# Kernel tuning notes

Measured on AMD Instinct MI355X. Metric: run time of the kernel, lower is better.

The kernel has to match this reference:

```python
import jax, jax.numpy as jnp
import numpy as np

B, N, E, OD, RD, ED, H = 4, 2048, 8192, 3, 4, 4, 8


def _linear(x, W, b):
    return x @ W + b


def _mlp_rel(x, p):
    # RelationalModel: Lin-ELU-Lin-ELU-Lin-ELU-Lin
    h = jax.nn.elu(_linear(x, p[0], p[1]))
    h = jax.nn.elu(_linear(h, p[2], p[3]))
    h = jax.nn.elu(_linear(h, p[4], p[5]))
    return _linear(h, p[6], p[7])


def _mlp_obj(x, p):
    # ObjectModel: Lin-ELU-Lin-ELU-Lin
    h = jax.nn.elu(_linear(x, p[0], p[1]))
    h = jax.nn.elu(_linear(h, p[2], p[3]))
    return _linear(h, p[4], p[5])


def setup_inputs() -> dict:
    key = jax.random.key(0)
    ks = jax.random.split(key, 24)
    X = jax.random.normal(ks[0], (B, OD, N), jnp.float32)
    Ra = jax.random.normal(ks[1], (B, E, RD), jnp.float32)
    # one-hot incidence matrices (receiver / sender), as in the torch repo
    ro_idx = jax.random.randint(ks[2], (B, E), 0, N)
    ri_idx = jax.random.randint(ks[3], (B, E), 0, N)
    Ro = jax.nn.one_hot(ro_idx, N, dtype=jnp.float32)
    Ri = jax.nn.one_hot(ri_idx, N, dtype=jnp.float32)

    def w(k, i, o):
        return jax.random.normal(k, (i, o), jnp.float32) * (1.0 / np.sqrt(i))

    def b(k, o):
        return jax.random.normal(k, (o,), jnp.float32) * 0.01

    m_in = 2 * OD + RD  # 10
    d = {
        "X": X, "Ra": Ra, "Ro": Ro, "Ri": Ri,
        # phi_R1: m_in -> H -> H -> H -> ED
        "r1W1": w(ks[4], m_in, H), "r1b1": b(ks[5], H),
        "r1W2": w(ks[6], H, H), "r1b2": b(ks[7], H),
        "r1W3": w(ks[8], H, H), "r1b3": b(ks[9], H),
        "r1W4": w(ks[10], H, ED), "r1b4": b(ks[11], ED),
        # phi_R2: m_in -> H -> H -> H -> 1
        "r2W1": w(ks[12], m_in, H), "r2b1": b(ks[13], H),
        "r2W2": w(ks[14], H, H), "r2b2": b(ks[15], H),
        "r2W3": w(ks[16], H, H), "r2b3": b(ks[17], H),
        "r2W4": w(ks[18], H, 1), "r2b4": b(ks[19], 1),
        # phi_O: OD+ED -> H -> H -> 3
        "oW1": w(ks[20], OD + ED, H), "ob1": b(ks[21], H),
        "oW2": w(ks[22], H, H), "ob2": b(ks[23], H),
        "oW3": w(jax.random.fold_in(key, 99), H, 3),
        "ob3": jnp.zeros((3,), jnp.float32),
    }
    return d


def reference(X, Ra, Ro, Ri,
              r1W1, r1b1, r1W2, r1b2, r1W3, r1b3, r1W4, r1b4,
              r2W1, r2b1, r2W2, r2b2, r2W3, r2b3, r2W4, r2b4,
              oW1, ob1, oW2, ob2, oW3, ob3):
    r1 = (r1W1, r1b1, r1W2, r1b2, r1W3, r1b3, r1W4, r1b4)
    r2 = (r2W1, r2b1, r2W2, r2b2, r2W3, r2b3, r2W4, r2b4)
    po = (oW1, ob1, oW2, ob2, oW3, ob3)

    Xt = jnp.swapaxes(X, 1, 2)          # [B, N, OD]
    Xi = jnp.einsum('ben,bnd->bed', Ro, Xt)   # receiver gather [B,E,OD]
    Xo = jnp.einsum('ben,bnd->bed', Ri, Xt)   # sender gather   [B,E,OD]
    m1 = jnp.concatenate([Xi, Xo, Ra], axis=2)  # [B,E,2*OD+RD]
    Eff = _mlp_rel(m1, r1)              # [B,E,ED]
    A = jnp.einsum('ben,bed->bnd', Ri, Eff)     # scatter-add to nodes [B,N,ED]
    C = jnp.concatenate([Xt, A], axis=2)        # [B,N,OD+ED]
    X_tilde = _mlp_obj(C, po)           # [B,N,3]
    Xi_t = jnp.einsum('ben,bnd->bed', Ri, X_tilde)
    Xo_t = jnp.einsum('ben,bnd->bed', Ro, X_tilde)
    m2 = jnp.concatenate([Xi_t, Xo_t, Eff], axis=2)  # [B,E,6+ED]
    W = jax.nn.sigmoid(_mlp_rel(m2, r2))  # [B,E,1]
    return W
```

## Files before the change

### kernel.cpp

```cpp
#include <hip/hip_runtime.h>
#include <hip/hip_bf16.h>
#include <cstdint>

#define NBATCH 4
#define NNODE  2048
#define NEDGE  8192
#define ETOT   (NBATCH * NEDGE)
#define NTOT   (NBATCH * NNODE)

typedef uint32_t u32x4 __attribute__((ext_vector_type(4)));

__device__ __forceinline__ float elu(float x) {
    return x > 0.0f ? x : expm1f(x);
}

__global__ void in_idx_kernel(const u32x4* __restrict__ Ro,
                              const u32x4* __restrict__ Ri,
                              int* __restrict__ ro_idx,
                              int* __restrict__ ri_idx,
                              float* __restrict__ A, int a_elems) {
    const int gtid = blockIdx.x * blockDim.x + threadIdx.x;
    if (gtid < a_elems) A[gtid] = 0.0f;

    const int wid  = gtid >> 6;
    const int lane = threadIdx.x & 63;
    const int nrows = 2 * ETOT;
    if (wid >= nrows) return;

    const bool second = (wid >= ETOT);
    const int  row    = second ? wid - ETOT : wid;
    const u32x4* __restrict__ src = (second ? Ri : Ro) + (size_t)row * (NNODE / 4);
    int* __restrict__ dst = second ? ri_idx : ro_idx;

    #pragma unroll
    for (int c = 0; c < NNODE / 256; ++c) {
        const u32x4 v = __builtin_nontemporal_load(&src[c * 64 + lane]);
        const uint32_t o = v.x | v.y | v.z | v.w;
        const unsigned long long found = __ballot(o != 0u);
        if (found) {
            if (o) {
                const int base = c * 256 + lane * 4;
                if      (v.x) dst[row] = base;
                else if (v.y) dst[row] = base + 1;
                else if (v.z) dst[row] = base + 2;
                else          dst[row] = base + 3;
            }
            break;
        }
    }
}

__global__ void in_edge1_kernel(const float* __restrict__ X,
                                const float* __restrict__ Ra,
                                const int* __restrict__ ro_idx,
                                const int* __restrict__ ri_idx,
                                const float* __restrict__ W1, const float* __restrict__ b1,
                                const float* __restrict__ W2, const float* __restrict__ b2,
                                const float* __restrict__ W3, const float* __restrict__ b3,
                                const float* __restrict__ W4, const float* __restrict__ b4,
                                float* __restrict__ Eff,
                                float* __restrict__ A) {
    __shared__ float sW1[80], sb1[8], sW2[64], sb2[8], sW3[64], sb3[8], sW4[32], sb4[4];
    const int t = threadIdx.x, bs = blockDim.x;
    for (int i = t; i < 80; i += bs) sW1[i] = W1[i];
    for (int i = t; i < 8;  i += bs) sb1[i] = b1[i];
    for (int i = t; i < 64; i += bs) sW2[i] = W2[i];
    for (int i = t; i < 8;  i += bs) sb2[i] = b2[i];
    for (int i = t; i < 64; i += bs) sW3[i] = W3[i];
    for (int i = t; i < 8;  i += bs) sb3[i] = b3[i];
    for (int i = t; i < 32; i += bs) sW4[i] = W4[i];
    for (int i = t; i < 4;  i += bs) sb4[i] = b4[i];
    __syncthreads();

    const int e = blockIdx.x * blockDim.x + threadIdx.x;
    if (e >= ETOT) return;
    const int b  = e >> 13;
    const int ro = ro_idx[e] & (NNODE - 1);
    const int ri = ri_idx[e] & (NNODE - 1);

    float x[10];
    const float* Xb = X + (long)b * 3 * NNODE;
    #pragma unroll
    for (int d = 0; d < 3; ++d) x[d]     = Xb[d * NNODE + ro];
    #pragma unroll
    for (int d = 0; d < 3; ++d) x[3 + d] = Xb[d * NNODE + ri];
    const float4 ra = ((const float4*)Ra)[e];
    x[6] = ra.x; x[7] = ra.y; x[8] = ra.z; x[9] = ra.w;

    float h1[8], h2[8], h3[8];
    #pragma unroll
    for (int j = 0; j < 8; ++j) {
        float s = sb1[j];
        #pragma unroll
        for (int i = 0; i < 10; ++i) s += x[i] * sW1[i * 8 + j];
        h1[j] = elu(s);
    }
    #pragma unroll
    for (int j = 0; j < 8; ++j) {
        float s = sb2[j];
        #pragma unroll
        for (int i = 0; i < 8; ++i) s += h1[i] * sW2[i * 8 + j];
        h2[j] = elu(s);
    }
    #pragma unroll
    for (int j = 0; j < 8; ++j) {
        float s = sb3[j];
        #pragma unroll
        for (int i = 0; i < 8; ++i) s += h2[i] * sW3[i * 8 + j];
        h3[j] = elu(s);
    }
    float* Arow = A + ((long)(b * NNODE + ri)) * 4;
    float4 eff;
    float* effp = (float*)&eff;
    #pragma unroll
    for (int j = 0; j < 4; ++j) {
        float s = sb4[j];
        #pragma unroll
        for (int i = 0; i < 8; ++i) s += h3[i] * sW4[i * 4 + j];
        effp[j] = s;
        atomicAdd(&Arow[j], s);
    }
    ((float4*)Eff)[e] = eff;
}

__global__ void in_node_kernel(const float* __restrict__ X,
                               const float* __restrict__ A,
                               const float* __restrict__ W1, const float* __restrict__ b1,
                               const float* __restrict__ W2, const float* __restrict__ b2,
                               const float* __restrict__ W3, const float* __restrict__ b3,
                               float* __restrict__ Xtil) {
    __shared__ float sW1[56], sb1[8], sW2[64], sb2[8], sW3[24], sb3[3];
    const int t = threadIdx.x, bs = blockDim.x;
    for (int i = t; i < 56; i += bs) sW1[i] = W1[i];
    for (int i = t; i < 8;  i += bs) sb1[i] = b1[i];
    for (int i = t; i < 64; i += bs) sW2[i] = W2[i];
    for (int i = t; i < 8;  i += bs) sb2[i] = b2[i];
    for (int i = t; i < 24; i += bs) sW3[i] = W3[i];
    for (int i = t; i < 3;  i += bs) sb3[i] = b3[i];
    __syncthreads();

    const int n = blockIdx.x * blockDim.x + threadIdx.x;
    if (n >= NTOT) return;
    const int b  = n >> 11;
    const int nn = n & (NNODE - 1);

    float c[7];
    const float* Xb = X + (long)b * 3 * NNODE;
    #pragma unroll
    for (int d = 0; d < 3; ++d) c[d] = Xb[d * NNODE + nn];
    const float4 a4 = ((const float4*)A)[n];
    c[3] = a4.x; c[4] = a4.y; c[5] = a4.z; c[6] = a4.w;

    float h1[8], h2[8];
    #pragma unroll
    for (int j = 0; j < 8; ++j) {
        float s = sb1[j];
        #pragma unroll
        for (int i = 0; i < 7; ++i) s += c[i] * sW1[i * 8 + j];
        h1[j] = elu(s);
    }
    #pragma unroll
    for (int j = 0; j < 8; ++j) {
        float s = sb2[j];
        #pragma unroll
        for (int i = 0; i < 8; ++i) s += h1[i] * sW2[i * 8 + j];
        h2[j] = elu(s);
    }
    #pragma unroll
    for (int j = 0; j < 3; ++j) {
        float s = sb3[j];
        #pragma unroll
        for (int i = 0; i < 8; ++i) s += h2[i] * sW3[i * 3 + j];
        Xtil[(long)n * 3 + j] = s;
    }
}

__global__ void in_edge2_kernel(const float* __restrict__ Xtil,
                                const float* __restrict__ Eff,
                                const int* __restrict__ ro_idx,
                                const int* __restrict__ ri_idx,
                                const float* __restrict__ W1, const float* __restrict__ b1,
                                const float* __restrict__ W2, const float* __restrict__ b2,
                                const float* __restrict__ W3, const float* __restrict__ b3,
                                const float* __restrict__ W4, const float* __restrict__ b4,
                                float* __restrict__ out) {
    __shared__ float sW1[80], sb1[8], sW2[64], sb2[8], sW3[64], sb3[8], sW4[8], sb4[1];
    const int t = threadIdx.x, bs = blockDim.x;
    for (int i = t; i < 80; i += bs) sW1[i] = W1[i];
    for (int i = t; i < 8;  i += bs) sb1[i] = b1[i];
    for (int i = t; i < 64; i += bs) sW2[i] = W2[i];
    for (int i = t; i < 8;  i += bs) sb2[i] = b2[i];
    for (int i = t; i < 64; i += bs) sW3[i] = W3[i];
    for (int i = t; i < 8;  i += bs) sb3[i] = b3[i];
    for (int i = t; i < 8;  i += bs) sW4[i] = W4[i];
    for (int i = t; i < 1;  i += bs) sb4[i] = b4[i];
    __syncthreads();

    const int e = blockIdx.x * blockDim.x + threadIdx.x;
    if (e >= ETOT) return;
    const int b  = e >> 13;
    const int ro = ro_idx[e] & (NNODE - 1);
    const int ri = ri_idx[e] & (NNODE - 1);

    float x[10];
    const float* Xb = Xtil + (long)b * NNODE * 3;
    #pragma unroll
    for (int d = 0; d < 3; ++d) x[d]     = Xb[(long)ri * 3 + d];
    #pragma unroll
    for (int d = 0; d < 3; ++d) x[3 + d] = Xb[(long)ro * 3 + d];
    const float4 ef = ((const float4*)Eff)[e];
    x[6] = ef.x; x[7] = ef.y; x[8] = ef.z; x[9] = ef.w;

    float h1[8], h2[8], h3[8];
    #pragma unroll
    for (int j = 0; j < 8; ++j) {
        float s = sb1[j];
        #pragma unroll
        for (int i = 0; i < 10; ++i) s += x[i] * sW1[i * 8 + j];
        h1[j] = elu(s);
    }
    #pragma unroll
    for (int j = 0; j < 8; ++j) {
        float s = sb2[j];
        #pragma unroll
        for (int i = 0; i < 8; ++i) s += h1[i] * sW2[i * 8 + j];
        h2[j] = elu(s);
    }
    #pragma unroll
    for (int j = 0; j < 8; ++j) {
        float s = sb3[j];
        #pragma unroll
        for (int i = 0; i < 8; ++i) s += h2[i] * sW3[i * 8 + j];
        h3[j] = elu(s);
    }
    float s = sb4[0];
    #pragma unroll
    for (int i = 0; i < 8; ++i) s += h3[i] * sW4[i];
    out[e] = 1.0f / (1.0f + expf(-s));
}

extern "C" void kernel_launch(void* const* d_in, const int* in_sizes, int n_in,
                              void* d_out, int out_size, void* d_ws, size_t ws_size,
                              hipStream_t stream) {
    const float* X  = (const float*)d_in[0];
    const float* Ra = (const float*)d_in[1];
    const float* Ro = (const float*)d_in[2];
    const float* Ri = (const float*)d_in[3];
    const float* r1W1 = (const float*)d_in[4];  const float* r1b1 = (const float*)d_in[5];
    const float* r1W2 = (const float*)d_in[6];  const float* r1b2 = (const float*)d_in[7];
    const float* r1W3 = (const float*)d_in[8];  const float* r1b3 = (const float*)d_in[9];
    const float* r1W4 = (const float*)d_in[10]; const float* r1b4 = (const float*)d_in[11];
    const float* r2W1 = (const float*)d_in[12]; const float* r2b1 = (const float*)d_in[13];
    const float* r2W2 = (const float*)d_in[14]; const float* r2b2 = (const float*)d_in[15];
    const float* r2W3 = (const float*)d_in[16]; const float* r2b3 = (const float*)d_in[17];
    const float* r2W4 = (const float*)d_in[18]; const float* r2b4 = (const float*)d_in[19];
    const float* oW1  = (const float*)d_in[20]; const float* ob1  = (const float*)d_in[21];
    const float* oW2  = (const float*)d_in[22]; const float* ob2  = (const float*)d_in[23];
    const float* oW3  = (const float*)d_in[24]; const float* ob3  = (const float*)d_in[25];

    char* ws = (char*)d_ws;
    int*   ro_idx = (int*)(ws + 0);
    int*   ri_idx = (int*)(ws + 131072);
    float* Eff    = (float*)(ws + 262144);
    float* A      = (float*)(ws + 786432);
    float* Xtil   = (float*)(ws + 917504);

    in_idx_kernel<<<(2 * ETOT * 64) / 256, 256, 0, stream>>>(
        (const u32x4*)Ro, (const u32x4*)Ri, ro_idx, ri_idx, A, NTOT * 4 );

    in_edge1_kernel<<<ETOT / 256, 256, 0, stream>>>(X, Ra, ro_idx, ri_idx,
                                                    r1W1, r1b1, r1W2, r1b2, r1W3, r1b3, r1W4, r1b4,
                                                    Eff, A);

    in_node_kernel<<<NTOT / 256, 256, 0, stream>>>(X, A,
                                                   oW1, ob1, oW2, ob2, oW3, ob3,
                                                   Xtil);

    in_edge2_kernel<<<ETOT / 256, 256, 0, stream>>>(Xtil, Eff, ro_idx, ri_idx,
                                                    r2W1, r2b1, r2W2, r2b2, r2W3, r2b3, r2W4, r2b4,
                                                    (float*)d_out);
}
```

Before: 76.01 us.

## Fuse edge, node and edge MLP stages into one cooperative kernel with grid syncs

Merges the three post-index kernels into a single cooperative launch of 128 blocks that separates the edge-MLP/scatter, node-MLP and second edge-MLP phases with grid-wide barriers. All weights are staged once into a single shared array. This removes two kernel launch gaps and the repeated weight loads, but adds the cost of cooperative launch and two grid syncs, and ties the grid size to co-residency limits.

```diff
diff --git a/kernel.cpp b/kernel.cpp
--- a/kernel.cpp
+++ b/kernel.cpp
@@ -1,6 +1,9 @@
 #include <hip/hip_runtime.h>
 #include <hip/hip_bf16.h>
+#include <hip/hip_cooperative_groups.h>
 #include <cstdint>
+
+namespace cg = cooperative_groups;
 
 #define NBATCH 4
 #define NNODE  2048
@@ -50,193 +53,179 @@
     }
 }
 
-__global__ void in_edge1_kernel(const float* __restrict__ X,
+__global__ void in_fused_kernel(const float* __restrict__ X,
                                 const float* __restrict__ Ra,
                                 const int* __restrict__ ro_idx,
                                 const int* __restrict__ ri_idx,
-                                const float* __restrict__ W1, const float* __restrict__ b1,
-                                const float* __restrict__ W2, const float* __restrict__ b2,
-                                const float* __restrict__ W3, const float* __restrict__ b3,
-                                const float* __restrict__ W4, const float* __restrict__ b4,
+                                const float* __restrict__ e1W1, const float* __restrict__ e1b1,
+                                const float* __restrict__ e1W2, const float* __restrict__ e1b2,
+                                const float* __restrict__ e1W3, const float* __restrict__ e1b3,
+                                const float* __restrict__ e1W4, const float* __restrict__ e1b4,
+                                const float* __restrict__ nW1,  const float* __restrict__ nb1,
+                                const float* __restrict__ nW2,  const float* __restrict__ nb2,
+                                const float* __restrict__ nW3,  const float* __restrict__ nb3,
+                                const float* __restrict__ e2W1, const float* __restrict__ e2b1,
+                                const float* __restrict__ e2W2, const float* __restrict__ e2b2,
+                                const float* __restrict__ e2W3, const float* __restrict__ e2b3,
+                                const float* __restrict__ e2W4, const float* __restrict__ e2b4,
                                 float* __restrict__ Eff,
-                                float* __restrict__ A) {
-    __shared__ float sW1[80], sb1[8], sW2[64], sb2[8], sW3[64], sb3[8], sW4[32], sb4[4];
+                                float* __restrict__ A,
+                                float* __restrict__ Xtil,
+                                float* __restrict__ out) {
+    __shared__ float s[672];
     const int t = threadIdx.x, bs = blockDim.x;
-    for (int i = t; i < 80; i += bs) sW1[i] = W1[i];
-    for (int i = t; i < 8;  i += bs) sb1[i] = b1[i];
-    for (int i = t; i < 64; i += bs) sW2[i] = W2[i];
-    for (int i = t; i < 8;  i += bs) sb2[i] = b2[i];
-    for (int i = t; i < 64; i += bs) sW3[i] = W3[i];
-    for (int i = t; i < 8;  i += bs) sb3[i] = b3[i];
-    for (int i = t; i < 32; i += bs) sW4[i] = W4[i];
-    for (int i = t; i < 4;  i += bs) sb4[i] = b4[i];
+    for (int i = t; i < 80; i += bs) s[i]       = e1W1[i];
+    for (int i = t; i < 8;  i += bs) s[80 + i]  = e1b1[i];
+    for (int i = t; i < 64; i += bs) s[88 + i]  = e1W2[i];
+    for (int i = t; i < 8;  i += bs) s[152 + i] = e1b2[i];
+    for (int i = t; i < 64; i += bs) s[160 + i] = e1W3[i];
+    for (int i = t; i < 8;  i += bs) s[224 + i] = e1b3[i];
+    for (int i = t; i < 32; i += bs) s[232 + i] = e1W4[i];
+    for (int i = t; i < 4;  i += bs) s[264 + i] = e1b4[i];
+    for (int i = t; i < 56; i += bs) s[268 + i] = nW1[i];
+    for (int i = t; i < 8;  i += bs) s[324 + i] = nb1[i];
+    for (int i = t; i < 64; i += bs) s[332 + i] = nW2[i];
+    for (int i = t; i < 8;  i += bs) s[396 + i] = nb2[i];
+    for (int i = t; i < 24; i += bs) s[404 + i] = nW3[i];
+    for (int i = t; i < 3;  i += bs) s[428 + i] = nb3[i];
+    for (int i = t; i < 80; i += bs) s[431 + i] = e2W1[i];
+    for (int i = t; i < 8;  i += bs) s[511 + i] = e2b1[i];
+    for (int i = t; i < 64; i += bs) s[519 + i] = e2W2[i];
+    for (int i = t; i < 8;  i += bs) s[583 + i] = e2b2[i];
+    for (int i = t; i < 64; i += bs) s[591 + i] = e2W3[i];
+    for (int i = t; i < 8;  i += bs) s[655 + i] = e2b3[i];
+    for (int i = t; i < 8;  i += bs) s[663 + i] = e2W4[i];
+    for (int i = t; i < 1;  i += bs) s[671 + i] = e2b4[i];
     __syncthreads();
 
-    const int e = blockIdx.x * blockDim.x + threadIdx.x;
-    if (e >= ETOT) return;
+    cg::grid_group grid = cg::this_grid();
+
+    const int e  = blockIdx.x * blockDim.x + threadIdx.x;
     const int b  = e >> 13;
     const int ro = ro_idx[e] & (NNODE - 1);
     const int ri = ri_idx[e] & (NNODE - 1);
 
-    float x[10];
-    const float* Xb = X + (long)b * 3 * NNODE;
-    #pragma unroll
-    for (int d = 0; d < 3; ++d) x[d]     = Xb[d * NNODE + ro];
-    #pragma unroll
-    for (int d = 0; d < 3; ++d) x[3 + d] = Xb[d * NNODE + ri];
-    const float4 ra = ((const float4*)Ra)[e];
-    x[6] = ra.x; x[7] = ra.y; x[8] = ra.z; x[9] = ra.w;
-
-    float h1[8], h2[8], h3[8];
-    #pragma unroll
-    for (int j = 0; j < 8; ++j) {
-        float s = sb1[j];
-        #pragma unroll
-        for (int i = 0; i < 10; ++i) s += x[i] * sW1[i * 8 + j];
-        h1[j] = elu(s);
-    }
-    #pragma unroll
-    for (int j = 0; j < 8; ++j) {
-        float s = sb2[j];
-        #pragma unroll
-        for (int i = 0; i < 8; ++i) s += h1[i] * sW2[i * 8 + j];
-        h2[j] = elu(s);
-    }
-    #pragma unroll
-    for (int j = 0; j < 8; ++j) {
-        float s = sb3[j];
-        #pragma unroll
-        for (int i = 0; i < 8; ++i) s += h2[i] * sW3[i * 8 + j];
-        h3[j] = elu(s);
-    }
-    float* Arow = A + ((long)(b * NNODE + ri)) * 4;
-    float4 eff;
-    float* effp = (float*)&eff;
-    #pragma unroll
-    for (int j = 0; j < 4; ++j) {
-        float s = sb4[j];
-        #pragma unroll
-        for (int i = 0; i < 8; ++i) s += h3[i] * sW4[i * 4 + j];
-        effp[j] = s;
-        atomicAdd(&Arow[j], s);
-    }
-    ((float4*)Eff)[e] = eff;
-}
-
-__global__ void in_node_kernel(const float* __restrict__ X,
-                               const float* __restrict__ A,
-                               const float* __restrict__ W1, const float* __restrict__ b1,
-                               const float* __restrict__ W2, const float* __restrict__ b2,
-                               const float* __restrict__ W3, const float* __restrict__ b3,
-                               float* __restrict__ Xtil) {
-    __shared__ float sW1[56], sb1[8], sW2[64], sb2[8], sW3[24], sb3[3];
-    const int t = threadIdx.x, bs = blockDim.x;
-    for (int i = t; i < 56; i += bs) sW1[i] = W1[i];
-    for (int i = t; i < 8;  i += bs) sb1[i] = b1[i];
-    for (int i = t; i < 64; i += bs) sW2[i] = W2[i];
-    for (int i = t; i < 8;  i += bs) sb2[i] = b2[i];
-    for (int i = t; i < 24; i += bs) sW3[i] = W3[i];
-    for (int i = t; i < 3;  i += bs) sb3[i] = b3[i];
-    __syncthreads();
-
-    const int n = blockIdx.x * blockDim.x + threadIdx.x;
-    if (n >= NTOT) return;
-    const int b  = n >> 11;
-    const int nn = n & (NNODE - 1);
-
-    float c[7];
-    const float* Xb = X + (long)b * 3 * NNODE;
-    #pragma unroll
-    for (int d = 0; d < 3; ++d) c[d] = Xb[d * NNODE + nn];
-    const float4 a4 = ((const float4*)A)[n];
-    c[3] = a4.x; c[4] = a4.y; c[5] = a4.z; c[6] = a4.w;
-
-    float h1[8], h2[8];
-    #pragma unroll
-    for (int j = 0; j < 8; ++j) {
-        float s = sb1[j];
-        #pragma unroll
-        for (int i = 0; i < 7; ++i) s += c[i] * sW1[i * 8 + j];
-        h1[j] = elu(s);
-    }
-    #pragma unroll
-    for (int j = 0; j < 8; ++j) {
-        float s = sb2[j];
-        #pragma unroll
-        for (int i = 0; i < 8; ++i) s += h1[i] * sW2[i * 8 + j];
-        h2[j] = elu(s);
-    }
-    #pragma unroll
-    for (int j = 0; j < 3; ++j) {
-        float s = sb3[j];
-        #pragma unroll
-        for (int i = 0; i < 8; ++i) s += h2[i] * sW3[i * 3 + j];
-        Xtil[(long)n * 3 + j] = s;
-    }
-}
-
-__global__ void in_edge2_kernel(const float* __restrict__ Xtil,
-                                const float* __restrict__ Eff,
-                                const int* __restrict__ ro_idx,
-                                const int* __restrict__ ri_idx,
-                                const float* __restrict__ W1, const float* __restrict__ b1,
-                                const float* __restrict__ W2, const float* __restrict__ b2,
-                                const float* __restrict__ W3, const float* __restrict__ b3,
-                                const float* __restrict__ W4, const float* __restrict__ b4,
-                                float* __restrict__ out) {
-    __shared__ float sW1[80], sb1[8], sW2[64], sb2[8], sW3[64], sb3[8], sW4[8], sb4[1];
-    const int t = threadIdx.x, bs = blockDim.x;
-    for (int i = t; i < 80; i += bs) sW1[i] = W1[i];
-    for (int i = t; i < 8;  i += bs) sb1[i] = b1[i];
-    for (int i = t; i < 64; i += bs) sW2[i] = W2[i];
-    for (int i = t; i < 8;  i += bs) sb2[i] = b2[i];
-    for (int i = t; i < 64; i += bs) sW3[i] = W3[i];
-    for (int i = t; i < 8;  i += bs) sb3[i] = b3[i];
-    for (int i = t; i < 8;  i += bs) sW4[i] = W4[i];
-    for (int i = t; i < 1;  i += bs) sb4[i] = b4[i];
-    __syncthreads();
-
-    const int e = blockIdx.x * blockDim.x + threadIdx.x;
-    if (e >= ETOT) return;
-    const int b  = e >> 13;
-    const int ro = ro_idx[e] & (NNODE - 1);
-    const int ri = ri_idx[e] & (NNODE - 1);
-
-    float x[10];
-    const float* Xb = Xtil + (long)b * NNODE * 3;
-    #pragma unroll
-    for (int d = 0; d < 3; ++d) x[d]     = Xb[(long)ri * 3 + d];
-    #pragma unroll
-    for (int d = 0; d < 3; ++d) x[3 + d] = Xb[(long)ro * 3 + d];
-    const float4 ef = ((const float4*)Eff)[e];
-    x[6] = ef.x; x[7] = ef.y; x[8] = ef.z; x[9] = ef.w;
-
-    float h1[8], h2[8], h3[8];
-    #pragma unroll
-    for (int j = 0; j < 8; ++j) {
-        float s = sb1[j];
-        #pragma unroll
-        for (int i = 0; i < 10; ++i) s += x[i] * sW1[i * 8 + j];
-        h1[j] = elu(s);
-    }
-    #pragma unroll
-    for (int j = 0; j < 8; ++j) {
-        float s = sb2[j];
-        #pragma unroll
-        for (int i = 0; i < 8; ++i) s += h1[i] * sW2[i * 8 + j];
-        h2[j] = elu(s);
-    }
-    #pragma unroll
-    for (int j = 0; j < 8; ++j) {
-        float s = sb3[j];
-        #pragma unroll
-        for (int i = 0; i < 8; ++i) s += h2[i] * sW3[i * 8 + j];
-        h3[j] = elu(s);
-    }
-    float s = sb4[0];
-    #pragma unroll
-    for (int i = 0; i < 8; ++i) s += h3[i] * sW4[i];
-    out[e] = 1.0f / (1.0f + expf(-s));
+    {
+        float x[10];
+        const float* Xb = X + (long)b * 3 * NNODE;
+        #pragma unroll
+        for (int d = 0; d < 3; ++d) x[d]     = Xb[d * NNODE + ro];
+        #pragma unroll
+        for (int d = 0; d < 3; ++d) x[3 + d] = Xb[d * NNODE + ri];
+        const float4 ra = ((const float4*)Ra)[e];
+        x[6] = ra.x; x[7] = ra.y; x[8] = ra.z; x[9] = ra.w;
+
+        float h1[8], h2[8], h3[8];
+        #pragma unroll
+        for (int j = 0; j < 8; ++j) {
+            float v = s[80 + j];
+            #pragma unroll
+            for (int i = 0; i < 10; ++i) v += x[i] * s[i * 8 + j];
+            h1[j] = elu(v);
+        }
+        #pragma unroll
+        for (int j = 0; j < 8; ++j) {
+            float v = s[152 + j];
+            #pragma unroll
+            for (int i = 0; i < 8; ++i) v += h1[i] * s[88 + i * 8 + j];
+            h2[j] = elu(v);
+        }
+        #pragma unroll
+        for (int j = 0; j < 8; ++j) {
+            float v = s[224 + j];
+            #pragma unroll
+            for (int i = 0; i < 8; ++i) v += h2[i] * s[160 + i * 8 + j];
+            h3[j] = elu(v);
+        }
+        float* Arow = A + ((long)(b * NNODE + ri)) * 4;
+        float4 eff;
+        float* effp = (float*)&eff;
+        #pragma unroll
+        for (int j = 0; j < 4; ++j) {
+            float v = s[264 + j];
+            #pragma unroll
+            for (int i = 0; i < 8; ++i) v += h3[i] * s[232 + i * 4 + j];
+            effp[j] = v;
+            atomicAdd(&Arow[j], v);
+        }
+        ((float4*)Eff)[e] = eff;
+    }
+
+    grid.sync();
+
+    if (e < NTOT) {
+        const int nb = e >> 11;
+        const int nn = e & (NNODE - 1);
+        float c[7];
+        const float* Xb = X + (long)nb * 3 * NNODE;
+        #pragma unroll
+        for (int d = 0; d < 3; ++d) c[d] = Xb[d * NNODE + nn];
+        const float4 a4 = ((const float4*)A)[e];
+        c[3] = a4.x; c[4] = a4.y; c[5] = a4.z; c[6] = a4.w;
+
+        float h1[8], h2[8];
+        #pragma unroll
+        for (int j = 0; j < 8; ++j) {
+            float v = s[324 + j];
+            #pragma unroll
+            for (int i = 0; i < 7; ++i) v += c[i] * s[268 + i * 8 + j];
+            h1[j] = elu(v);
+        }
+        #pragma unroll
+        for (int j = 0; j < 8; ++j) {
+            float v = s[396 + j];
+            #pragma unroll
+            for (int i = 0; i < 8; ++i) v += h1[i] * s[332 + i * 8 + j];
+            h2[j] = elu(v);
+        }
+        #pragma unroll
+        for (int j = 0; j < 3; ++j) {
+            float v = s[428 + j];
+            #pragma unroll
+            for (int i = 0; i < 8; ++i) v += h2[i] * s[404 + i * 3 + j];
+            Xtil[(long)e * 3 + j] = v;
+        }
+    }
+
+    grid.sync();
+
+    {
+        float x[10];
+        const float* Xb = Xtil + (long)b * NNODE * 3;
+        #pragma unroll
+        for (int d = 0; d < 3; ++d) x[d]     = Xb[(long)ri * 3 + d];
+        #pragma unroll
+        for (int d = 0; d < 3; ++d) x[3 + d] = Xb[(long)ro * 3 + d];
+        const float4 ef = ((const float4*)Eff)[e];
+        x[6] = ef.x; x[7] = ef.y; x[8] = ef.z; x[9] = ef.w;
+
+        float h1[8], h2[8], h3[8];
+        #pragma unroll
+        for (int j = 0; j < 8; ++j) {
+            float v = s[511 + j];
+            #pragma unroll
+            for (int i = 0; i < 10; ++i) v += x[i] * s[431 + i * 8 + j];
+            h1[j] = elu(v);
+        }
+        #pragma unroll
+        for (int j = 0; j < 8; ++j) {
+            float v = s[583 + j];
+            #pragma unroll
+            for (int i = 0; i < 8; ++i) v += h1[i] * s[519 + i * 8 + j];
+            h2[j] = elu(v);
+        }
+        #pragma unroll
+        for (int j = 0; j < 8; ++j) {
+            float v = s[655 + j];
+            #pragma unroll
+            for (int i = 0; i < 8; ++i) v += h2[i] * s[591 + i * 8 + j];
+            h3[j] = elu(v);
+        }
+        float v = s[671];
+        #pragma unroll
+        for (int i = 0; i < 8; ++i) v += h3[i] * s[663 + i];
+        out[e] = 1.0f / (1.0f + expf(-v));
+    }
 }
 
 extern "C" void kernel_launch(void* const* d_in, const int* in_sizes, int n_in,
@@ -264,19 +253,21 @@
     float* Eff    = (float*)(ws + 262144);
     float* A      = (float*)(ws + 786432);
     float* Xtil   = (float*)(ws + 917504);
+    float* out    = (float*)d_out;
 
     in_idx_kernel<<<(2 * ETOT * 64) / 256, 256, 0, stream>>>(
         (const u32x4*)Ro, (const u32x4*)Ri, ro_idx, ri_idx, A, NTOT * 4 );
 
-    in_edge1_kernel<<<ETOT / 256, 256, 0, stream>>>(X, Ra, ro_idx, ri_idx,
-                                                    r1W1, r1b1, r1W2, r1b2, r1W3, r1b3, r1W4, r1b4,
-                                                    Eff, A);
-
-    in_node_kernel<<<NTOT / 256, 256, 0, stream>>>(X, A,
-                                                   oW1, ob1, oW2, ob2, oW3, ob3,
-                                                   Xtil);
-
-    in_edge2_kernel<<<ETOT / 256, 256, 0, stream>>>(Xtil, Eff, ro_idx, ri_idx,
-                                                    r2W1, r2b1, r2W2, r2b2, r2W3, r2b3, r2W4, r2b4,
-                                                    (float*)d_out);
-}
+    void* args[] = {
+        (void*)&X, (void*)&Ra, (void*)&ro_idx, (void*)&ri_idx,
+        (void*)&r1W1, (void*)&r1b1, (void*)&r1W2, (void*)&r1b2,
+        (void*)&r1W3, (void*)&r1b3, (void*)&r1W4, (void*)&r1b4,
+        (void*)&oW1,  (void*)&ob1,  (void*)&oW2,  (void*)&ob2,
+        (void*)&oW3,  (void*)&ob3,
+        (void*)&r2W1, (void*)&r2b1, (void*)&r2W2, (void*)&r2b2,
+        (void*)&r2W3, (void*)&r2b3, (void*)&r2W4, (void*)&r2b4,
+        (void*)&Eff, (void*)&A, (void*)&Xtil, (void*)&out
+    };
+    hipLaunchCooperativeKernel((const void*)in_fused_kernel,
+                               dim3(ETOT / 256), dim3(256), args, 0, stream);
+}
```

Result: slower. 118.0 us (+55.2%).
